# Performance work log

Measured on AMD Instinct MI355X. Metric: run time of the kernel, lower is better.

Reference implementation:

```python
import jax, jax.numpy as jnp
import numpy as np

B, C, W, H = 4, 256, 64, 64

def setup_inputs() -> dict:
    key = jax.random.key(0)
    ks = jax.random.split(key, 6)
    return {
        "fm_source": jax.random.normal(ks[0], (B, C, W, H), dtype=jnp.float32),
        "fm_reference": jax.random.normal(ks[1], (B, C, W, H), dtype=jnp.float32),
        "w_lambda": jax.random.normal(ks[2], (1, C, 1, 1), dtype=jnp.float32) * 0.05,
        "b_lambda": jax.random.normal(ks[3], (1,), dtype=jnp.float32) * 0.05,
        "w_beta": jax.random.normal(ks[4], (1, C, 1, 1), dtype=jnp.float32) * 0.05,
        "b_beta": jax.random.normal(ks[5], (1,), dtype=jnp.float32) * 0.05,
    }

def reference(fm_source, fm_reference, w_lambda, b_lambda, w_beta, b_beta):
    b, c, w, h = fm_reference.shape
    n = w * h
    # 1x1 convs on the reference feature map -> per-pixel scalars, flattened to [B, N]
    wl = w_lambda.reshape(c)
    wb = w_beta.reshape(c)
    ref_flat = fm_reference.reshape(b, c, n)   # [B, C, N]
    src_flat = fm_source.reshape(b, c, n)      # [B, C, N]
    old_lambda = jnp.einsum("bcn,c->bn", ref_flat, wl) + b_lambda[0]  # [B, N]
    old_beta = jnp.einsum("bcn,c->bn", ref_flat, wb) + b_beta[0]      # [B, N]
    # energy[b, i, j] = <src pixel i, ref pixel j> over channels
    energy = jnp.einsum("bci,bcj->bij", src_flat, ref_flat)  # [B, N, N]
    attention = jax.nn.softmax(energy, axis=-1)              # softmax over ref pixels j
    # new_lambda[b, i] = sum_j old_lambda[b, j] * attention[b, i, j]
    new_lambda = jnp.einsum("bj,bij->bi", old_lambda, attention).reshape(b, 1, w, h)
    new_beta = jnp.einsum("bj,bij->bi", old_beta, attention).reshape(b, 1, w, h)
    # broadcast modulation over the 256 channels
    return new_lambda * fm_source + new_beta
```

## Files before the change

### kernel.cpp

```cpp
#include <hip/hip_runtime.h>


#define B_ 4
#define C_ 256
#define N_ 4096
#define LOG2E 1.44269504f
#define SHIFT2 86.5617f
#define JSLICE 8
#define BN_ (B_ * N_)
#define NT_ 16
#define PH_ 8

typedef _Float16 half_t;
typedef _Float16 v8h  __attribute__((ext_vector_type(8)));
typedef float    v16f __attribute__((ext_vector_type(16)));

#define GLDS16(g, l) __builtin_amdgcn_global_load_lds(                         \
    (const __attribute__((address_space(1))) void*)(g),                        \
    (__attribute__((address_space(3))) void*)(l), 16, 0, 0)

__global__ void k_prep(const float* __restrict__ src,
                       const float* __restrict__ ref,
                       const float* __restrict__ wl,
                       const float* __restrict__ wb,
                       half_t* __restrict__ s16, half_t* __restrict__ r16,
                       float* __restrict__ oldLp, float* __restrict__ oldBp,
                       float* __restrict__ sums ) {
    __shared__ float tile[64][65];
    __shared__ float red[8][64];
    int z  = blockIdx.z;
    int isRef = z >> 2;
    int b  = z & 3;
    const float* in  = isRef ? ref : src;
    half_t*      out = isRef ? r16 : s16;
    float scale      = isRef ? 1.0f : LOG2E;
    int c0 = blockIdx.y * 64;
    int n0 = blockIdx.x * 64;
    int tid = threadIdx.x;
    if (z == 0) {
        int gid = (blockIdx.y * 64 + blockIdx.x) * 256 + tid;
        if (gid < 3 * BN_) sums[gid] = 0.f;
    }
    int tx = tid & 15, ty = tid >> 4;
#pragma unroll
    for (int q = 0; q < 4; q++) {
        int c = ty + q * 16;
        float4 v = *(const float4*)(in + ((size_t)b * C_ + c0 + c) * N_ + n0 + tx * 4);
        tile[c][tx * 4 + 0] = v.x;
        tile[c][tx * 4 + 1] = v.y;
        tile[c][tx * 4 + 2] = v.z;
        tile[c][tx * 4 + 3] = v.w;
    }
    __syncthreads();
    int r   = tid & 31;
    int lhi = (tid >> 5) & 1;
    int wv  = tid >> 6;
#pragma unroll
    for (int nt = 0; nt < 2; nt++) {
        int nl = nt * 32 + r;
        v8h o;
#pragma unroll
        for (int e = 0; e < 8; e++)
            o[e] = (half_t)(tile[wv * 16 + lhi * 8 + e][nl] * scale);
        size_t tj = (size_t)(n0 >> 5) + nt;
        size_t kb = (size_t)(c0 >> 4) + wv;
        *(v8h*)(out + ((((size_t)b * 128 + tj) * 16 + kb) * 64 + (tid & 63)) * 8) = o;
    }
    if (!isRef) return;
    int n  = tid & 63;
    int cq = tid >> 6;
    float aL = 0.f, aB = 0.f;
#pragma unroll
    for (int c = 0; c < 16; c++) {
        float v = tile[cq * 16 + c][n];
        aL += v * wl[c0 + cq * 16 + c];
        aB += v * wb[c0 + cq * 16 + c];
    }
    red[cq][n]     = aL;
    red[4 + cq][n] = aB;
    __syncthreads();
    size_t slot = ((size_t)blockIdx.y * B_ + b) * N_ + n0;
    if (tid < 64) {
        oldLp[slot + tid] = red[0][tid] + red[1][tid] + red[2][tid] + red[3][tid];
    } else if (tid < 128) {
        int u = tid - 64;
        oldBp[slot + u] = red[4][u] + red[5][u] + red[6][u] + red[7][u];
    }
}

__global__ __launch_bounds__(512, 2) void k_flash(
        const half_t* __restrict__ sT, const half_t* __restrict__ rT,
        const float* __restrict__ oldLp, const float* __restrict__ oldBp,
        const float* __restrict__ bl, const float* __restrict__ bb,
        float* __restrict__ sumP, float* __restrict__ sumL,
        float* __restrict__ sumB) {
    __shared__ half_t lds[2][16384];
    int bid    = blockIdx.x;
    int b      = bid & 3;
    int jslice = (bid >> 2) & (JSLICE - 1);
    int iblock = bid >> 5;
    int tid    = threadIdx.x;
    int wv     = tid >> 6;
    int lane   = tid & 63;
    int l31    = lane & 31, lhi = lane >> 5;
    int ti     = iblock * 8 + wv;
    int i0     = ti * 32;
    int j0     = jslice * (N_ / JSLICE);
    int tj0    = j0 >> 5;

    const half_t* aP = sT + (((size_t)b * 128 + ti) * 16) * 512 + (size_t)lane * 8;
    v8h a[16];
#pragma unroll
    for (int kb = 0; kb < 16; kb++) a[kb] = *(const v8h*)(aP + (size_t)kb * 512);

    const half_t* bBase = rT + (((size_t)b * 128 + tj0) * 16) * 512;
    const float*  oLp = oldLp + (size_t)b * N_ + j0 + l31;
    const float*  oBp = oldBp + (size_t)b * N_ + j0 + l31;
    float bl0 = bl[0], bb0 = bb[0];

    float sp[16], sl[16], sb[16];
#pragma unroll
    for (int r = 0; r < 16; r++) { sp[r] = 0.f; sl[r] = 0.f; sb[r] = 0.f; }

#pragma unroll
    for (int q = 0; q < 4; q++) {
        int chunk = q * 8 + wv;
        GLDS16(bBase + (size_t)chunk * 512 + (size_t)lane * 8,
               &lds[0][(size_t)chunk * 512]);
    }

    for (int ph = 0; ph < PH_; ph++) {
        __syncthreads();
        if (ph + 1 < PH_) {
            const half_t* g = bBase + (size_t)(ph + 1) * 16384;
#pragma unroll
            for (int q = 0; q < 4; q++) {
                int chunk = q * 8 + wv;
                GLDS16(g + (size_t)chunk * 512 + (size_t)lane * 8,
                       &lds[(ph + 1) & 1][(size_t)chunk * 512]);
            }
        }
#pragma unroll
        for (int t = 0; t < 2; t++) {
            int jt = ph * 2 + t;
            const half_t* bt = lds[ph & 1] + (size_t)t * 8192 + (size_t)lane * 8;
            float lam = oLp[jt * 32]           + oLp[BN_ + jt * 32]
                      + oLp[2 * BN_ + jt * 32] + oLp[3 * BN_ + jt * 32] + bl0;
            float bet = oBp[jt * 32]           + oBp[BN_ + jt * 32]
                      + oBp[2 * BN_ + jt * 32] + oBp[3 * BN_ + jt * 32] + bb0;
            v16f acc0, acc1;
#pragma unroll
            for (int r = 0; r < 16; r++) { acc0[r] = -SHIFT2; acc1[r] = 0.f; }
#pragma unroll
            for (int kb = 0; kb < 8; kb++) {
                acc0 = __builtin_amdgcn_mfma_f32_32x32x16_f16(
                    a[kb],     *(const v8h*)(bt + (size_t)kb * 512),       acc0, 0, 0, 0);
                acc1 = __builtin_amdgcn_mfma_f32_32x32x16_f16(
                    a[kb + 8], *(const v8h*)(bt + (size_t)(kb + 8) * 512), acc1, 0, 0, 0);
            }
#pragma unroll
            for (int r = 0; r < 16; r++) {
                float p = __builtin_amdgcn_exp2f(acc0[r] + acc1[r]);
                sp[r] += p;
                sl[r] += p * lam;
                sb[r] += p * bet;
            }
        }
    }

#pragma unroll
    for (int r = 0; r < 16; r++) {
        float tp = sp[r], tl = sl[r], tb = sb[r];
#pragma unroll
        for (int m = 1; m <= 16; m <<= 1) {
            tp += __shfl_xor(tp, m, 64);
            tl += __shfl_xor(tl, m, 64);
            tb += __shfl_xor(tb, m, 64);
        }
        if (l31 == 0) {
            int row = (r & 3) + 8 * (r >> 2) + 4 * lhi;
            size_t ig = (size_t)b * N_ + i0 + row;
            atomicAdd(&sumP[ig], tp);
            atomicAdd(&sumL[ig], tl);
            atomicAdd(&sumB[ig], tb);
        }
    }
}

__global__ void k_post(const float* __restrict__ src,
                       const float* __restrict__ sums,
                       float* __restrict__ out) {
    int b  = blockIdx.x;
    int n0 = blockIdx.y * 1024;
    int c0 = blockIdx.z * 4;
    int t  = threadIdx.x;
    size_t bn = (size_t)b * N_ + n0 + t * 4;
    float4 sp = *(const float4*)(sums + bn);
    float4 sl = *(const float4*)(sums + BN_ + bn);
    float4 sb = *(const float4*)(sums + 2 * BN_ + bn);
    float4 L, T;
    L.x = sl.x / sp.x; L.y = sl.y / sp.y; L.z = sl.z / sp.z; L.w = sl.w / sp.w;
    T.x = sb.x / sp.x; T.y = sb.y / sp.y; T.z = sb.z / sp.z; T.w = sb.w / sp.w;
    const float* sp0 = src + ((size_t)b * C_ + c0) * N_ + n0 + t * 4;
    float*       op0 = out + ((size_t)b * C_ + c0) * N_ + n0 + t * 4;
#pragma unroll
    for (int c = 0; c < 4; c++) {
        float4 v = *(const float4*)(sp0 + (size_t)c * N_);
        float4 o;
        o.x = L.x * v.x + T.x;
        o.y = L.y * v.y + T.y;
        o.z = L.z * v.z + T.z;
        o.w = L.w * v.w + T.w;
        *(float4*)(op0 + (size_t)c * N_) = o;
    }
}

extern "C" void kernel_launch(void* const* d_in, const int* in_sizes, int n_in,
                              void* d_out, int out_size, void* d_ws, size_t ws_size,
                              hipStream_t stream) {
    const float* src = (const float*)d_in[0];
    const float* ref = (const float*)d_in[1];
    const float* wl  = (const float*)d_in[2];
    const float* bl  = (const float*)d_in[3];
    const float* wb  = (const float*)d_in[4];
    const float* bb  = (const float*)d_in[5];
    float* out = (float*)d_out;

    float* oldLp = (float*)d_ws;
    float* oldBp = oldLp + 4 * BN_;
    float* sums  = oldBp + 4 * BN_;
    float* sumP  = sums;
    float* sumL  = sums + BN_;
    float* sumB  = sums + 2 * BN_;
    size_t needF  = (size_t)11 * BN_ * sizeof(float);
    size_t need16 = (size_t)2 * B_ * N_ * C_ * sizeof(half_t);
    half_t* s16;
    if (ws_size >= needF + need16) s16 = (half_t*)((char*)d_ws + needF);
    else                           s16 = (half_t*)d_out;
    half_t* r16 = s16 + (size_t)B_ * N_ * C_;

    k_prep<<<dim3(N_ / 64, C_ / 64, 8), 256, 0, stream>>>(
        src, ref, wl, wb, s16, r16, oldLp, oldBp, sums);
    k_flash<<<B_ * JSLICE * 16, 512, 0, stream>>>(
        s16, r16, oldLp, oldBp, bl, bb, sumP, sumL, sumB);
    k_post<<<dim3(B_, N_ / 1024, C_ / 4), 256, 0, stream>>>(src, sums, out);
}
```

Baseline: 149.9 us.

## Fuse source fp16 conversion into flash kernel and stage lambda/beta in LDS

```diff
diff --git a/kernel.cpp b/kernel.cpp
--- a/kernel.cpp
+++ b/kernel.cpp
@@ -9,7 +9,6 @@
 #define JSLICE 8
 #define BN_ (B_ * N_)
 #define NT_ 16
-#define PH_ 8
 
 typedef _Float16 half_t;
 typedef _Float16 v8h  __attribute__((ext_vector_type(8)));
@@ -19,25 +18,19 @@
     (const __attribute__((address_space(1))) void*)(g),                        \
     (__attribute__((address_space(3))) void*)(l), 16, 0, 0)
 
-__global__ void k_prep(const float* __restrict__ src,
-                       const float* __restrict__ ref,
+__global__ void k_prep(const float* __restrict__ ref,
                        const float* __restrict__ wl,
                        const float* __restrict__ wb,
-                       half_t* __restrict__ s16, half_t* __restrict__ r16,
+                       half_t* __restrict__ r16,
                        float* __restrict__ oldLp, float* __restrict__ oldBp,
                        float* __restrict__ sums ) {
     __shared__ float tile[64][65];
     __shared__ float red[8][64];
-    int z  = blockIdx.z;
-    int isRef = z >> 2;
-    int b  = z & 3;
-    const float* in  = isRef ? ref : src;
-    half_t*      out = isRef ? r16 : s16;
-    float scale      = isRef ? 1.0f : LOG2E;
+    int b  = blockIdx.z;
     int c0 = blockIdx.y * 64;
     int n0 = blockIdx.x * 64;
     int tid = threadIdx.x;
-    if (z == 0) {
+    if (b == 0) {
         int gid = (blockIdx.y * 64 + blockIdx.x) * 256 + tid;
         if (gid < 3 * BN_) sums[gid] = 0.f;
     }
@@ -45,7 +38,7 @@
 #pragma unroll
     for (int q = 0; q < 4; q++) {
         int c = ty + q * 16;
-        float4 v = *(const float4*)(in + ((size_t)b * C_ + c0 + c) * N_ + n0 + tx * 4);
+        float4 v = *(const float4*)(ref + ((size_t)b * C_ + c0 + c) * N_ + n0 + tx * 4);
         tile[c][tx * 4 + 0] = v.x;
         tile[c][tx * 4 + 1] = v.y;
         tile[c][tx * 4 + 2] = v.z;
@@ -61,12 +54,11 @@
         v8h o;
 #pragma unroll
         for (int e = 0; e < 8; e++)
-            o[e] = (half_t)(tile[wv * 16 + lhi * 8 + e][nl] * scale);
+            o[e] = (half_t)tile[wv * 16 + lhi * 8 + e][nl];
         size_t tj = (size_t)(n0 >> 5) + nt;
         size_t kb = (size_t)(c0 >> 4) + wv;
-        *(v8h*)(out + ((((size_t)b * 128 + tj) * 16 + kb) * 64 + (tid & 63)) * 8) = o;
-    }
-    if (!isRef) return;
+        *(v8h*)(r16 + ((((size_t)b * 128 + tj) * 16 + kb) * 64 + (tid & 63)) * 8) = o;
+    }
     int n  = tid & 63;
     int cq = tid >> 6;
     float aL = 0.f, aB = 0.f;
@@ -89,12 +81,13 @@
 }
 
 __global__ __launch_bounds__(512, 2) void k_flash(
-        const half_t* __restrict__ sT, const half_t* __restrict__ rT,
+        const float* __restrict__ src, const half_t* __restrict__ rT,
         const float* __restrict__ oldLp, const float* __restrict__ oldBp,
         const float* __restrict__ bl, const float* __restrict__ bb,
         float* __restrict__ sumP, float* __restrict__ sumL,
         float* __restrict__ sumB) {
-    __shared__ half_t lds[2][16384];
+    __shared__ half_t lds[2][8192];
+    __shared__ float oL[512], oB[512];
     int bid    = blockIdx.x;
     int b      = bid & 3;
     int jslice = (bid >> 2) & (JSLICE - 1);
@@ -108,63 +101,72 @@
     int j0     = jslice * (N_ / JSLICE);
     int tj0    = j0 >> 5;
 
-    const half_t* aP = sT + (((size_t)b * 128 + ti) * 16) * 512 + (size_t)lane * 8;
+    const float* aS = src + (size_t)b * C_ * N_ + i0 + l31;
     v8h a[16];
 #pragma unroll
-    for (int kb = 0; kb < 16; kb++) a[kb] = *(const v8h*)(aP + (size_t)kb * 512);
+    for (int kb = 0; kb < 16; kb++) {
+        v8h o;
+#pragma unroll
+        for (int e = 0; e < 8; e++)
+            o[e] = (half_t)(aS[(size_t)(kb * 16 + lhi * 8 + e) * N_] * LOG2E);
+        a[kb] = o;
+    }
+
+    {
+        float accL = bl[0], accB = bb[0];
+        size_t base = (size_t)b * N_ + j0 + tid;
+#pragma unroll
+        for (int g = 0; g < 4; g++) {
+            accL += oldLp[(size_t)g * BN_ + base];
+            accB += oldBp[(size_t)g * BN_ + base];
+        }
+        oL[tid] = accL;
+        oB[tid] = accB;
+    }
 
     const half_t* bBase = rT + (((size_t)b * 128 + tj0) * 16) * 512;
-    const float*  oLp = oldLp + (size_t)b * N_ + j0 + l31;
-    const float*  oBp = oldBp + (size_t)b * N_ + j0 + l31;
-    float bl0 = bl[0], bb0 = bb[0];
 
     float sp[16], sl[16], sb[16];
 #pragma unroll
     for (int r = 0; r < 16; r++) { sp[r] = 0.f; sl[r] = 0.f; sb[r] = 0.f; }
 
 #pragma unroll
-    for (int q = 0; q < 4; q++) {
+    for (int q = 0; q < 2; q++) {
         int chunk = q * 8 + wv;
         GLDS16(bBase + (size_t)chunk * 512 + (size_t)lane * 8,
                &lds[0][(size_t)chunk * 512]);
     }
 
-    for (int ph = 0; ph < PH_; ph++) {
+    for (int jt = 0; jt < NT_; jt++) {
         __syncthreads();
-        if (ph + 1 < PH_) {
-            const half_t* g = bBase + (size_t)(ph + 1) * 16384;
-#pragma unroll
-            for (int q = 0; q < 4; q++) {
+        if (jt + 1 < NT_) {
+            const half_t* g = bBase + (size_t)(jt + 1) * 8192;
+#pragma unroll
+            for (int q = 0; q < 2; q++) {
                 int chunk = q * 8 + wv;
                 GLDS16(g + (size_t)chunk * 512 + (size_t)lane * 8,
-                       &lds[(ph + 1) & 1][(size_t)chunk * 512]);
+                       &lds[(jt + 1) & 1][(size_t)chunk * 512]);
             }
         }
-#pragma unroll
-        for (int t = 0; t < 2; t++) {
-            int jt = ph * 2 + t;
-            const half_t* bt = lds[ph & 1] + (size_t)t * 8192 + (size_t)lane * 8;
-            float lam = oLp[jt * 32]           + oLp[BN_ + jt * 32]
-                      + oLp[2 * BN_ + jt * 32] + oLp[3 * BN_ + jt * 32] + bl0;
-            float bet = oBp[jt * 32]           + oBp[BN_ + jt * 32]
-                      + oBp[2 * BN_ + jt * 32] + oBp[3 * BN_ + jt * 32] + bb0;
-            v16f acc0, acc1;
-#pragma unroll
-            for (int r = 0; r < 16; r++) { acc0[r] = -SHIFT2; acc1[r] = 0.f; }
-#pragma unroll
-            for (int kb = 0; kb < 8; kb++) {
-                acc0 = __builtin_amdgcn_mfma_f32_32x32x16_f16(
-                    a[kb],     *(const v8h*)(bt + (size_t)kb * 512),       acc0, 0, 0, 0);
-                acc1 = __builtin_amdgcn_mfma_f32_32x32x16_f16(
-                    a[kb + 8], *(const v8h*)(bt + (size_t)(kb + 8) * 512), acc1, 0, 0, 0);
-            }
-#pragma unroll
-            for (int r = 0; r < 16; r++) {
-                float p = __builtin_amdgcn_exp2f(acc0[r] + acc1[r]);
-                sp[r] += p;
-                sl[r] += p * lam;
-                sb[r] += p * bet;
-            }
+        const half_t* bt = lds[jt & 1] + (size_t)lane * 8;
+        float lam = oL[jt * 32 + l31];
+        float bet = oB[jt * 32 + l31];
+        v16f acc0, acc1;
+#pragma unroll
+        for (int r = 0; r < 16; r++) { acc0[r] = -SHIFT2; acc1[r] = 0.f; }
+#pragma unroll
+        for (int kb = 0; kb < 8; kb++) {
+            acc0 = __builtin_amdgcn_mfma_f32_32x32x16_f16(
+                a[kb],     *(const v8h*)(bt + (size_t)kb * 512),       acc0, 0, 0, 0);
+            acc1 = __builtin_amdgcn_mfma_f32_32x32x16_f16(
+                a[kb + 8], *(const v8h*)(bt + (size_t)(kb + 8) * 512), acc1, 0, 0, 0);
+        }
+#pragma unroll
+        for (int r = 0; r < 16; r++) {
+            float p = __builtin_amdgcn_exp2f(acc0[r] + acc1[r]);
+            sp[r] += p;
+            sl[r] += p * lam;
+            sb[r] += p * bet;
         }
     }
 
@@ -233,15 +235,14 @@
     float* sumL  = sums + BN_;
     float* sumB  = sums + 2 * BN_;
     size_t needF  = (size_t)11 * BN_ * sizeof(float);
-    size_t need16 = (size_t)2 * B_ * N_ * C_ * sizeof(half_t);
-    half_t* s16;
-    if (ws_size >= needF + need16) s16 = (half_t*)((char*)d_ws + needF);
-    else                           s16 = (half_t*)d_out;
-    half_t* r16 = s16 + (size_t)B_ * N_ * C_;
-
-    k_prep<<<dim3(N_ / 64, C_ / 64, 8), 256, 0, stream>>>(
-        src, ref, wl, wb, s16, r16, oldLp, oldBp, sums);
+    size_t need16 = (size_t)B_ * N_ * C_ * sizeof(half_t);
+    half_t* r16;
+    if (ws_size >= needF + need16) r16 = (half_t*)((char*)d_ws + needF);
+    else                           r16 = (half_t*)d_out;
+
+    k_prep<<<dim3(N_ / 64, C_ / 64, B_), 256, 0, stream>>>(
+        ref, wl, wb, r16, oldLp, oldBp, sums);
     k_flash<<<B_ * JSLICE * 16, 512, 0, stream>>>(
-        s16, r16, oldLp, oldBp, bl, bb, sumP, sumL, sumB);
+        src, r16, oldLp, oldBp, bl, bb, sumP, sumL, sumB);
     k_post<<<dim3(B_, N_ / 1024, C_ / 4), 256, 0, stream>>>(src, sums, out);
 }
```

New measurement: 151.2 us. Within noise of the previous version (+0.9%).

## Software-pipeline exp/accumulate of previous tile with MFMA of current tile

Applied to the files above, without the earlier changes.

```diff
diff --git a/kernel.cpp b/kernel.cpp
--- a/kernel.cpp
+++ b/kernel.cpp
@@ -9,7 +9,6 @@
 #define JSLICE 8
 #define BN_ (B_ * N_)
 #define NT_ 16
-#define PH_ 8
 
 typedef _Float16 half_t;
 typedef _Float16 v8h  __attribute__((ext_vector_type(8)));
@@ -18,6 +17,39 @@
 #define GLDS16(g, l) __builtin_amdgcn_global_load_lds(                         \
     (const __attribute__((address_space(1))) void*)(g),                        \
     (__attribute__((address_space(3))) void*)(l), 16, 0, 0)
+
+#define TILE_SEC(T, ACC0, ACC1, LAM, BET, DO_FIN, FACC0, FACC1, FLAM, FBET)    \
+  {                                                                            \
+    __syncthreads();                                                           \
+    if ((T) + 1 < NT_) {                                                       \
+      const half_t* g = bBase + (size_t)((T) + 1) * 8192;                      \
+      _Pragma("unroll")                                                        \
+      for (int q = 0; q < 2; q++) {                                            \
+        int chunk = q * 8 + wv;                                                \
+        GLDS16(g + (size_t)chunk * 512 + (size_t)lane * 8,                     \
+               &lds[((T) + 1) & 1][(size_t)chunk * 512]);                      \
+      }                                                                        \
+    }                                                                          \
+    LAM = oL[(T) * 32 + l31];                                                  \
+    BET = oB[(T) * 32 + l31];                                                  \
+    const half_t* bt = lds[(T) & 1] + (size_t)lane * 8;                        \
+    _Pragma("unroll")                                                          \
+    for (int r = 0; r < 16; r++) { ACC0[r] = -SHIFT2; ACC1[r] = 0.f; }         \
+    _Pragma("unroll")                                                          \
+    for (int kb = 0; kb < 8; kb++) {                                           \
+      ACC0 = __builtin_amdgcn_mfma_f32_32x32x16_f16(                           \
+          a[kb], *(const v8h*)(bt + (size_t)kb * 512), ACC0, 0, 0, 0);         \
+      ACC1 = __builtin_amdgcn_mfma_f32_32x32x16_f16(                           \
+          a[kb + 8], *(const v8h*)(bt + (size_t)(kb + 8) * 512), ACC1, 0,0,0); \
+      if (DO_FIN) {                                                            \
+        _Pragma("unroll")                                                      \
+        for (int rr = 2 * kb; rr < 2 * kb + 2; rr++) {                         \
+          float p = __builtin_amdgcn_exp2f(FACC0[rr] + FACC1[rr]);             \
+          sp[rr] += p; sl[rr] += p * FLAM; sb[rr] += p * FBET;                 \
+        }                                                                      \
+      }                                                                        \
+    }                                                                          \
+  }
 
 __global__ void k_prep(const float* __restrict__ src,
                        const float* __restrict__ ref,
@@ -94,7 +126,8 @@
         const float* __restrict__ bl, const float* __restrict__ bb,
         float* __restrict__ sumP, float* __restrict__ sumL,
         float* __restrict__ sumB) {
-    __shared__ half_t lds[2][16384];
+    __shared__ half_t lds[2][8192];
+    __shared__ float oL[512], oB[512];
     int bid    = blockIdx.x;
     int b      = bid & 3;
     int jslice = (bid >> 2) & (JSLICE - 1);
@@ -113,59 +146,45 @@
 #pragma unroll
     for (int kb = 0; kb < 16; kb++) a[kb] = *(const v8h*)(aP + (size_t)kb * 512);
 
+    {
+        float accL = bl[0], accB = bb[0];
+        size_t base = (size_t)b * N_ + j0 + tid;
+#pragma unroll
+        for (int g = 0; g < 4; g++) {
+            accL += oldLp[(size_t)g * BN_ + base];
+            accB += oldBp[(size_t)g * BN_ + base];
+        }
+        oL[tid] = accL;
+        oB[tid] = accB;
+    }
+
     const half_t* bBase = rT + (((size_t)b * 128 + tj0) * 16) * 512;
-    const float*  oLp = oldLp + (size_t)b * N_ + j0 + l31;
-    const float*  oBp = oldBp + (size_t)b * N_ + j0 + l31;
-    float bl0 = bl[0], bb0 = bb[0];
 
     float sp[16], sl[16], sb[16];
 #pragma unroll
     for (int r = 0; r < 16; r++) { sp[r] = 0.f; sl[r] = 0.f; sb[r] = 0.f; }
 
 #pragma unroll
-    for (int q = 0; q < 4; q++) {
+    for (int q = 0; q < 2; q++) {
         int chunk = q * 8 + wv;
         GLDS16(bBase + (size_t)chunk * 512 + (size_t)lane * 8,
                &lds[0][(size_t)chunk * 512]);
     }
 
-    for (int ph = 0; ph < PH_; ph++) {
-        __syncthreads();
-        if (ph + 1 < PH_) {
-            const half_t* g = bBase + (size_t)(ph + 1) * 16384;
-#pragma unroll
-            for (int q = 0; q < 4; q++) {
-                int chunk = q * 8 + wv;
-                GLDS16(g + (size_t)chunk * 512 + (size_t)lane * 8,
-                       &lds[(ph + 1) & 1][(size_t)chunk * 512]);
-            }
-        }
-#pragma unroll
-        for (int t = 0; t < 2; t++) {
-            int jt = ph * 2 + t;
-            const half_t* bt = lds[ph & 1] + (size_t)t * 8192 + (size_t)lane * 8;
-            float lam = oLp[jt * 32]           + oLp[BN_ + jt * 32]
-                      + oLp[2 * BN_ + jt * 32] + oLp[3 * BN_ + jt * 32] + bl0;
-            float bet = oBp[jt * 32]           + oBp[BN_ + jt * 32]
-                      + oBp[2 * BN_ + jt * 32] + oBp[3 * BN_ + jt * 32] + bb0;
-            v16f acc0, acc1;
-#pragma unroll
-            for (int r = 0; r < 16; r++) { acc0[r] = -SHIFT2; acc1[r] = 0.f; }
-#pragma unroll
-            for (int kb = 0; kb < 8; kb++) {
-                acc0 = __builtin_amdgcn_mfma_f32_32x32x16_f16(
-                    a[kb],     *(const v8h*)(bt + (size_t)kb * 512),       acc0, 0, 0, 0);
-                acc1 = __builtin_amdgcn_mfma_f32_32x32x16_f16(
-                    a[kb + 8], *(const v8h*)(bt + (size_t)(kb + 8) * 512), acc1, 0, 0, 0);
-            }
-#pragma unroll
-            for (int r = 0; r < 16; r++) {
-                float p = __builtin_amdgcn_exp2f(acc0[r] + acc1[r]);
-                sp[r] += p;
-                sl[r] += p * lam;
-                sb[r] += p * bet;
-            }
-        }
+    v16f accA0, accA1, accB0, accB1;
+    float lamA = 0.f, betA = 0.f, lamB = 0.f, betB = 0.f;
+
+    TILE_SEC(0, accA0, accA1, lamA, betA, false, accB0, accB1, lamB, betB)
+    for (int pt = 0; pt < 7; pt++) {
+        int t1 = 2 * pt + 1, t2 = 2 * pt + 2;
+        TILE_SEC(t1, accB0, accB1, lamB, betB, true, accA0, accA1, lamA, betA)
+        TILE_SEC(t2, accA0, accA1, lamA, betA, true, accB0, accB1, lamB, betB)
+    }
+    TILE_SEC(15, accB0, accB1, lamB, betB, true, accA0, accA1, lamA, betA)
+#pragma unroll
+    for (int r = 0; r < 16; r++) {
+        float p = __builtin_amdgcn_exp2f(accB0[r] + accB1[r]);
+        sp[r] += p; sl[r] += p * lamB; sb[r] += p * betB;
     }
 
 #pragma unroll
```

After: 148.1 us. About the same (-1.1%).
